# Kernel optimization log

Measured on AMD Instinct MI355X. Metric: run time of the kernel, lower is better.

## Reference

```python
import jax, jax.numpy as jnp
import numpy as np

N_NODES = 100000
N_EDGES = 1600000
RBF_DIM = 64
DIM = 64


def shifted_softplus(x):
    # torch.nn.Softplus(beta=0.5, threshold=14): (1/0.5)*log(1+exp(0.5*x)),
    # with linear passthrough when 0.5*x > 14.
    half = 0.5 * x
    return jnp.where(half > 14.0, x, 2.0 * jnp.logaddexp(0.0, half))


def setup_inputs() -> dict:
    key = jax.random.key(0)
    ks = jax.random.split(key, 8)
    node_weight = jax.random.normal(ks[0], (N_NODES, DIM), dtype=jnp.float32)
    rbf_out = jax.random.normal(ks[1], (N_EDGES, RBF_DIM), dtype=jnp.float32)
    # Linear params (torch Linear: y = x @ W.T + b); store W already transposed as (in,out)
    s1 = 1.0 / np.sqrt(RBF_DIM)
    s2 = 1.0 / np.sqrt(DIM)
    W1 = jax.random.uniform(ks[2], (RBF_DIM, DIM), jnp.float32, -s1, s1)
    b1 = jax.random.uniform(ks[3], (DIM,), jnp.float32, -s1, s1)
    W2 = jax.random.uniform(ks[4], (DIM, DIM), jnp.float32, -s2, s2)
    b2 = jax.random.uniform(ks[5], (DIM,), jnp.float32, -s2, s2)
    src = jax.random.randint(ks[6], (N_EDGES,), 0, N_NODES, dtype=jnp.int32)
    dst = jax.random.randint(ks[7], (N_EDGES,), 0, N_NODES, dtype=jnp.int32)
    return {
        "node_weight": node_weight, "rbf_out": rbf_out,
        "W1": W1, "b1": b1, "W2": W2, "b2": b2,
        "src": src, "dst": dst, "n_nodes": N_NODES,
    }


def reference(node_weight, rbf_out, W1, b1, W2, b2, src, dst, n_nodes):
    # edge MLP: Linear -> shifted softplus -> Linear, on rbf features  [E, dim]
    e = shifted_softplus(rbf_out @ W1 + b1) @ W2 + b2
    # gather source node weight per edge, multiply by edge filter      [E, dim]
    m = node_weight[src] * e
    # scatter-sum messages into destination nodes                      [N, dim]
    h = jax.ops.segment_sum(m, dst, num_segments=n_nodes)
    return h
```

## Files before the change

### kernel.cpp

```cpp
#include <hip/hip_runtime.h>
#include <math.h>

typedef short bf16x8 __attribute__((ext_vector_type(8)));
typedef float f32x4 __attribute__((ext_vector_type(4)));

__device__ __forceinline__ short f2bf(float f) {
    union { float f; unsigned u; } v; v.f = f;
    unsigned r = v.u + 0x7fffu + ((v.u >> 16) & 1u);
    return (short)(r >> 16);
}

__device__ __forceinline__ float ssp(float x) {
    float h = 0.5f * x;
    return 2.0f * (fmaxf(h, 0.0f) + __logf(1.0f + __expf(-fabsf(h))));
}

__global__ __launch_bounds__(256, 2) void cfconv_kernel(
    const float* __restrict__ nw, const float* __restrict__ rbf,
    const float* __restrict__ W1, const float* __restrict__ b1,
    const float* __restrict__ W2, const float* __restrict__ b2,
    const int* __restrict__ src, const int* __restrict__ dst,
    float* __restrict__ out, int n_edges)
{
    __shared__ __align__(16) short lds_h[4][16 * 72];

    const int tid  = threadIdx.x;
    const int wave = tid >> 6;
    const int lane = tid & 63;
    const int l16  = lane & 15;
    const int quad = lane >> 4;

    bf16x8 w1f[2][4], w2f[2][4];
    #pragma unroll
    for (int ks = 0; ks < 2; ++ks) {
        #pragma unroll
        for (int nt = 0; nt < 4; ++nt) {
            const int col = l16 + 16 * nt;
            const int k0  = quad * 8 + 32 * ks;
            bf16x8 a, b;
            #pragma unroll
            for (int j = 0; j < 8; ++j) {
                a[j] = f2bf(W1[(k0 + j) * 64 + col]);
                b[j] = f2bf(W2[(k0 + j) * 64 + col]);
            }
            w1f[ks][nt] = a;
            w2f[ks][nt] = b;
        }
    }
    float b1v[4], b2v[4];
    #pragma unroll
    for (int nt = 0; nt < 4; ++nt) {
        b1v[nt] = b1[l16 + 16 * nt];
        b2v[nt] = b2[l16 + 16 * nt];
    }

    short* myh = lds_h[wave];
    const int ntiles = (n_edges + 15) >> 4;
    const int gw = blockIdx.x * 4 + wave;
    const int stride = gridDim.x * 4;

    for (int t = gw; t < ntiles; t += stride) {
        const int e0 = t * 16;

        int arow = e0 + l16;
        if (arow >= n_edges) arow = n_edges - 1;
        const float* rp = rbf + (size_t)arow * 64 + quad * 8;
        bf16x8 af[2];
        #pragma unroll
        for (int ks = 0; ks < 2; ++ks) {
            float4 lo = *(const float4*)(rp + 32 * ks);
            float4 hi = *(const float4*)(rp + 32 * ks + 4);
            bf16x8 a;
            a[0] = f2bf(lo.x); a[1] = f2bf(lo.y); a[2] = f2bf(lo.z); a[3] = f2bf(lo.w);
            a[4] = f2bf(hi.x); a[5] = f2bf(hi.y); a[6] = f2bf(hi.z); a[7] = f2bf(hi.w);
            af[ks] = a;
        }

        f32x4 acc[4] = { {0.f,0.f,0.f,0.f}, {0.f,0.f,0.f,0.f},
                         {0.f,0.f,0.f,0.f}, {0.f,0.f,0.f,0.f} };
        #pragma unroll
        for (int nt = 0; nt < 4; ++nt)
            #pragma unroll
            for (int ks = 0; ks < 2; ++ks)
                acc[nt] = __builtin_amdgcn_mfma_f32_16x16x32_bf16(
                    af[ks], w1f[ks][nt], acc[nt], 0, 0, 0);

        #pragma unroll
        for (int nt = 0; nt < 4; ++nt)
            #pragma unroll
            for (int r = 0; r < 4; ++r)
                myh[(quad * 4 + r) * 72 + l16 + 16 * nt] =
                    f2bf(ssp(acc[nt][r] + b1v[nt]));

        bf16x8 hf[2];
        #pragma unroll
        for (int ks = 0; ks < 2; ++ks)
            hf[ks] = *(const bf16x8*)(myh + l16 * 72 + quad * 8 + 32 * ks);

        f32x4 acc2[4] = { {0.f,0.f,0.f,0.f}, {0.f,0.f,0.f,0.f},
                          {0.f,0.f,0.f,0.f}, {0.f,0.f,0.f,0.f} };
        #pragma unroll
        for (int nt = 0; nt < 4; ++nt)
            #pragma unroll
            for (int ks = 0; ks < 2; ++ks)
                acc2[nt] = __builtin_amdgcn_mfma_f32_16x16x32_bf16(
                    hf[ks], w2f[ks][nt], acc2[nt], 0, 0, 0);

        #pragma unroll
        for (int r = 0; r < 4; ++r) {
            const int e = e0 + quad * 4 + r;
            if (e < n_edges) {
                const int s = src[e], d = dst[e];
                const float* nwp = nw + (size_t)s * 64;
                float* op = out + (size_t)d * 64;
                #pragma unroll
                for (int nt = 0; nt < 4; ++nt) {
                    const int col = l16 + 16 * nt;
                    atomicAdd(op + col, (acc2[nt][r] + b2v[nt]) * nwp[col]);
                }
            }
        }
    }
}

extern "C" void kernel_launch(void* const* d_in, const int* in_sizes, int n_in,
                              void* d_out, int out_size, void* d_ws, size_t ws_size,
                              hipStream_t stream) {
    const float* nw  = (const float*)d_in[0];
    const float* rbf = (const float*)d_in[1];
    const float* W1  = (const float*)d_in[2];
    const float* b1  = (const float*)d_in[3];
    const float* W2  = (const float*)d_in[4];
    const float* b2  = (const float*)d_in[5];
    const int*   src = (const int*)d_in[6];
    const int*   dst = (const int*)d_in[7];
    float* out = (float*)d_out;
    const int n_edges = in_sizes[6];

    hipMemsetAsync(out, 0, (size_t)out_size * sizeof(float), stream);

    const int blocks = 1024;
    hipLaunchKernelGGL(cfconv_kernel, dim3(blocks), dim3(256), 0, stream,
                       nw, rbf, W1, b1, W2, b2, src, dst, out, n_edges);
}
```

Measured before the change: 807.5 us.

## Sort edges by destination into CSR and gather per node instead of atomics

Adds a counting sort on every call: histogram of dst, a multi-kernel prefix scan, and an atomic-cursor scatter that builds an edge permutation grouped by destination node. A new kernel gives each wave one destination node. It runs the two-layer edge MLP on that node's edges in tiles of 16, reduces the messages in registers with shuffles, and writes each output row once. This replaces the roughly hundred million float atomicAdds on the output and the zeroing memset. The costs are several extra small launches, random rbf row reads through the permutation, and idle MFMA lanes when a node's edge count is not a multiple of 16. The new path needs enough workspace and falls back to the old atomic kernel otherwise.

```diff
diff --git a/kernel.cpp b/kernel.cpp
--- a/kernel.cpp
+++ b/kernel.cpp
@@ -13,6 +13,197 @@
 __device__ __forceinline__ float ssp(float x) {
     float h = 0.5f * x;
     return 2.0f * (fmaxf(h, 0.0f) + __logf(1.0f + __expf(-fabsf(h))));
+}
+
+__global__ void hist_kernel(const int* __restrict__ dst, int* __restrict__ counts,
+                            int n_edges) {
+    int i = blockIdx.x * blockDim.x + threadIdx.x;
+    int gs = gridDim.x * blockDim.x;
+    for (int e = i; e < n_edges; e += gs) atomicAdd(&counts[dst[e]], 1);
+}
+
+__global__ __launch_bounds__(256) void scan_blocks(const int* __restrict__ counts,
+        int* __restrict__ base, int* __restrict__ partials, int n) {
+    __shared__ int wsum[4];
+    const int tid = threadIdx.x, lane = tid & 63, wv = tid >> 6;
+    const int i0 = blockIdx.x * 1024 + tid * 4;
+    int c[4], ts = 0;
+    #pragma unroll
+    for (int j = 0; j < 4; ++j) { c[j] = (i0 + j < n) ? counts[i0 + j] : 0; ts += c[j]; }
+    int x = ts;
+    #pragma unroll
+    for (int off = 1; off < 64; off <<= 1) {
+        int y = __shfl_up(x, off);
+        if (lane >= off) x += y;
+    }
+    if (lane == 63) wsum[wv] = x;
+    __syncthreads();
+    int woff = 0;
+    for (int w = 0; w < wv; ++w) woff += wsum[w];
+    int run = woff + x - ts;
+    #pragma unroll
+    for (int j = 0; j < 4; ++j) { if (i0 + j < n) base[i0 + j] = run; run += c[j]; }
+    if (tid == 255) partials[blockIdx.x] = woff + x;
+}
+
+__global__ void scan_partials(int* __restrict__ partials, int nblk) {
+    const int lane = threadIdx.x;
+    int carry = 0;
+    for (int b = 0; b < nblk; b += 64) {
+        const int i = b + lane;
+        int v = (i < nblk) ? partials[i] : 0;
+        int x = v;
+        #pragma unroll
+        for (int off = 1; off < 64; off <<= 1) {
+            int y = __shfl_up(x, off);
+            if (lane >= off) x += y;
+        }
+        if (i < nblk) partials[i] = carry + x - v;
+        carry += __shfl(x, 63);
+    }
+}
+
+__global__ __launch_bounds__(256) void add_offsets(int* __restrict__ base,
+        const int* __restrict__ partials, int n, int total) {
+    const int i0 = blockIdx.x * 1024 + threadIdx.x * 4;
+    const int p = partials[blockIdx.x];
+    #pragma unroll
+    for (int j = 0; j < 4; ++j) if (i0 + j < n) base[i0 + j] += p;
+    if (blockIdx.x == 0 && threadIdx.x == 0) base[n] = total;
+}
+
+__global__ void scatter_kernel(const int* __restrict__ dst, const int* __restrict__ base,
+        int* __restrict__ cursor, int* __restrict__ perm, int n_edges) {
+    int i = blockIdx.x * blockDim.x + threadIdx.x;
+    int gs = gridDim.x * blockDim.x;
+    for (int e = i; e < n_edges; e += gs) {
+        int d = dst[e];
+        int off = atomicAdd(&cursor[d], 1);
+        perm[base[d] + off] = e;
+    }
+}
+
+__global__ __launch_bounds__(256, 2) void cfconv_gather(
+    const float* __restrict__ nw, const float* __restrict__ rbf,
+    const float* __restrict__ W1, const float* __restrict__ b1,
+    const float* __restrict__ W2, const float* __restrict__ b2,
+    const int* __restrict__ src,
+    const int* __restrict__ perm, const int* __restrict__ base,
+    float* __restrict__ out, int n_nodes)
+{
+    __shared__ __align__(16) short lds_h[4][16 * 72];
+
+    const int tid  = threadIdx.x;
+    const int wave = tid >> 6;
+    const int lane = tid & 63;
+    const int l16  = lane & 15;
+    const int quad = lane >> 4;
+
+    bf16x8 w1f[2][4], w2f[2][4];
+    #pragma unroll
+    for (int ks = 0; ks < 2; ++ks) {
+        #pragma unroll
+        for (int nt = 0; nt < 4; ++nt) {
+            const int col = l16 + 16 * nt;
+            const int k0  = quad * 8 + 32 * ks;
+            bf16x8 a, b;
+            #pragma unroll
+            for (int j = 0; j < 8; ++j) {
+                a[j] = f2bf(W1[(k0 + j) * 64 + col]);
+                b[j] = f2bf(W2[(k0 + j) * 64 + col]);
+            }
+            w1f[ks][nt] = a;
+            w2f[ks][nt] = b;
+        }
+    }
+    float b1v[4], b2v[4];
+    #pragma unroll
+    for (int nt = 0; nt < 4; ++nt) {
+        b1v[nt] = b1[l16 + 16 * nt];
+        b2v[nt] = b2[l16 + 16 * nt];
+    }
+
+    short* myh = lds_h[wave];
+    const int gw = blockIdx.x * 4 + wave;
+    const int stride = gridDim.x * 4;
+
+    for (int n = gw; n < n_nodes; n += stride) {
+        const int s0 = base[n], s1 = base[n + 1];
+        float hsum[4] = {0.f, 0.f, 0.f, 0.f};
+
+        for (int p = s0; p < s1; p += 16) {
+            const int v = s1 - p;
+
+            const int e_a = perm[(l16 < v) ? (p + l16) : p];
+            const float* rp = rbf + (size_t)e_a * 64 + quad * 8;
+            bf16x8 af[2];
+            #pragma unroll
+            for (int ks = 0; ks < 2; ++ks) {
+                float4 lo = *(const float4*)(rp + 32 * ks);
+                float4 hi = *(const float4*)(rp + 32 * ks + 4);
+                bf16x8 a;
+                a[0] = f2bf(lo.x); a[1] = f2bf(lo.y); a[2] = f2bf(lo.z); a[3] = f2bf(lo.w);
+                a[4] = f2bf(hi.x); a[5] = f2bf(hi.y); a[6] = f2bf(hi.z); a[7] = f2bf(hi.w);
+                af[ks] = a;
+            }
+
+            f32x4 acc[4] = { {0.f,0.f,0.f,0.f}, {0.f,0.f,0.f,0.f},
+                             {0.f,0.f,0.f,0.f}, {0.f,0.f,0.f,0.f} };
+            #pragma unroll
+            for (int nt = 0; nt < 4; ++nt)
+                #pragma unroll
+                for (int ks = 0; ks < 2; ++ks)
+                    acc[nt] = __builtin_amdgcn_mfma_f32_16x16x32_bf16(
+                        af[ks], w1f[ks][nt], acc[nt], 0, 0, 0);
+
+            #pragma unroll
+            for (int nt = 0; nt < 4; ++nt)
+                #pragma unroll
+                for (int r = 0; r < 4; ++r)
+                    myh[(quad * 4 + r) * 72 + l16 + 16 * nt] =
+                        f2bf(ssp(acc[nt][r] + b1v[nt]));
+
+            bf16x8 hf[2];
+            #pragma unroll
+            for (int ks = 0; ks < 2; ++ks)
+                hf[ks] = *(const bf16x8*)(myh + l16 * 72 + quad * 8 + 32 * ks);
+
+            f32x4 acc2[4] = { {0.f,0.f,0.f,0.f}, {0.f,0.f,0.f,0.f},
+                              {0.f,0.f,0.f,0.f}, {0.f,0.f,0.f,0.f} };
+            #pragma unroll
+            for (int nt = 0; nt < 4; ++nt)
+                #pragma unroll
+                for (int ks = 0; ks < 2; ++ks)
+                    acc2[nt] = __builtin_amdgcn_mfma_f32_16x16x32_bf16(
+                        hf[ks], w2f[ks][nt], acc2[nt], 0, 0, 0);
+
+            #pragma unroll
+            for (int r = 0; r < 4; ++r) {
+                const int q = quad * 4 + r;
+                if (q < v) {
+                    const int e = perm[p + q];
+                    const int s = src[e];
+                    const float* nwp = nw + (size_t)s * 64;
+                    #pragma unroll
+                    for (int nt = 0; nt < 4; ++nt)
+                        hsum[nt] += (acc2[nt][r] + b2v[nt]) * nwp[l16 + 16 * nt];
+                }
+            }
+        }
+
+        #pragma unroll
+        for (int nt = 0; nt < 4; ++nt) {
+            float x = hsum[nt];
+            x += __shfl_xor(x, 16);
+            x += __shfl_xor(x, 32);
+            hsum[nt] = x;
+        }
+        float o = hsum[0];
+        o = (quad == 1) ? hsum[1] : o;
+        o = (quad == 2) ? hsum[2] : o;
+        o = (quad == 3) ? hsum[3] : o;
+        out[(size_t)n * 64 + quad * 16 + l16] = o;
+    }
 }
 
 __global__ __launch_bounds__(256, 2) void cfconv_kernel(
@@ -61,7 +252,6 @@
 
     for (int t = gw; t < ntiles; t += stride) {
         const int e0 = t * 16;
-
         int arow = e0 + l16;
         if (arow >= n_edges) arow = n_edges - 1;
         const float* rp = rbf + (size_t)arow * 64 + quad * 8;
@@ -136,10 +326,40 @@
     const int*   dst = (const int*)d_in[7];
     float* out = (float*)d_out;
     const int n_edges = in_sizes[6];
-
-    hipMemsetAsync(out, 0, (size_t)out_size * sizeof(float), stream);
-
-    const int blocks = 1024;
-    hipLaunchKernelGGL(cfconv_kernel, dim3(blocks), dim3(256), 0, stream,
-                       nw, rbf, W1, b1, W2, b2, src, dst, out, n_edges);
-}
+    const int n_nodes = out_size / 64;
+
+    const size_t need = ((size_t)(n_nodes + 1) + (size_t)n_nodes + 1024 + (size_t)n_edges)
+                        * sizeof(int);
+
+    if (ws_size >= need) {
+        int* base     = (int*)d_ws;
+        int* counts   = base + (n_nodes + 1);
+        int* partials = counts + n_nodes;
+        int* perm     = partials + 1024;
+
+        const int nblk = (n_nodes + 1023) / 1024;
+        int eblocks = (n_edges + 255) / 256;
+        if (eblocks > 8192) eblocks = 8192;
+
+        hipMemsetAsync(counts, 0, (size_t)n_nodes * sizeof(int), stream);
+        hipLaunchKernelGGL(hist_kernel, dim3(eblocks), dim3(256), 0, stream,
+                           dst, counts, n_edges);
+        hipLaunchKernelGGL(scan_blocks, dim3(nblk), dim3(256), 0, stream,
+                           counts, base, partials, n_nodes);
+        hipLaunchKernelGGL(scan_partials, dim3(1), dim3(64), 0, stream,
+                           partials, nblk);
+        hipLaunchKernelGGL(add_offsets, dim3(nblk), dim3(256), 0, stream,
+                           base, partials, n_nodes, n_edges);
+        hipMemsetAsync(counts, 0, (size_t)n_nodes * sizeof(int), stream);
+        hipLaunchKernelGGL(scatter_kernel, dim3(eblocks), dim3(256), 0, stream,
+                           dst, base, counts, perm, n_edges);
+
+        const int nodeblocks = (n_nodes + 3) / 4;
+        hipLaunchKernelGGL(cfconv_gather, dim3(nodeblocks), dim3(256), 0, stream,
+                           nw, rbf, W1, b1, W2, b2, src, perm, base, out, n_nodes);
+    } else {
+        hipMemsetAsync(out, 0, (size_t)out_size * sizeof(float), stream);
+        hipLaunchKernelGGL(cfconv_kernel, dim3(1024), dim3(256), 0, stream,
+                           nw, rbf, W1, b1, W2, b2, src, dst, out, n_edges);
+    }
+}
```

Result: slower. 1.086 ms (+34.5%).
